# Kernel tuning notes

Measured on AMD Instinct MI355X. Metric: run time of the kernel, lower is better.

Reference implementation:

```python
import jax, jax.numpy as jnp
import numpy as np

NUM_BUCKETS = 32
MAX_DISTANCE = 128


def _relative_position_bucket(relative_position):
    # bidirectional=True variant of T5's bucketing
    n = -relative_position
    num_buckets = NUM_BUCKETS // 2
    ret = (n < 0).astype(jnp.int32) * num_buckets
    n = jnp.abs(n)
    max_exact = num_buckets // 2
    is_small = n < max_exact
    # log-spaced buckets for large distances
    val_if_large = max_exact + (
        jnp.log(jnp.maximum(n, 1).astype(jnp.float32) / max_exact)
        / np.log(MAX_DISTANCE / max_exact)
        * (num_buckets - max_exact)
    ).astype(jnp.int32)
    val_if_large = jnp.minimum(val_if_large, num_buckets - 1)
    return ret + jnp.where(is_small, n, val_if_large)


def setup_inputs() -> dict:
    key = jax.random.key(0)
    ks = jax.random.split(key, 6)
    B, S, D, H, DK = 4, 1024, 1024, 16, 64
    inner = H * DK
    s = 1.0 / np.sqrt(D).astype(np.float32)
    x = jax.random.normal(ks[0], (B, S, D), jnp.float32)
    Wq = jax.random.normal(ks[1], (D, inner), jnp.float32) * s
    Wk = jax.random.normal(ks[2], (D, inner), jnp.float32) * s
    Wv = jax.random.normal(ks[3], (D, inner), jnp.float32) * s
    Wo = jax.random.normal(ks[4], (inner, D), jnp.float32) * s
    rel_emb = jax.random.normal(ks[5], (NUM_BUCKETS, H), jnp.float32) * 0.02
    return {"x": x, "Wq": Wq, "Wk": Wk, "Wv": Wv, "Wo": Wo, "rel_emb": rel_emb}


def reference(x, Wq, Wk, Wv, Wo, rel_emb):
    B, S, D = x.shape
    H = rel_emb.shape[1]
    DK = Wq.shape[1] // H

    def shape_heads(t):  # [B,S,H*DK] -> [B,H,S,DK]
        return t.reshape(B, S, H, DK).transpose(0, 2, 1, 3)

    q = shape_heads(x @ Wq)
    k = shape_heads(x @ Wk)
    v = shape_heads(x @ Wv)

    # note: T5 does NOT scale by 1/sqrt(d_kv)
    scores = jnp.einsum("bhqd,bhkd->bhqk", q, k)

    pos = jnp.arange(S)
    rel = pos[None, :] - pos[:, None]            # memory - query
    bucket = _relative_position_bucket(rel)      # [S,S] int32
    bias = rel_emb[bucket].transpose(2, 0, 1)[None]  # [1,H,S,S]

    weights = jax.nn.softmax(scores + bias, axis=-1)
    ctx = jnp.einsum("bhqk,bhkd->bhqd", weights, v)
    ctx = ctx.transpose(0, 2, 1, 3).reshape(B, S, H * DK)
    return ctx @ Wo
```

## Files before the change

### kernel.cpp

```cpp
#include <hip/hip_runtime.h>
#include <math.h>

#define B_ 4
#define S_ 1024
#define D_ 1024
#define H_ 16
#define DK_ 64

typedef short bf16x8 __attribute__((ext_vector_type(8)));
typedef float f32x4 __attribute__((ext_vector_type(4)));

__device__ __forceinline__ unsigned short f2bf(float f) {
    unsigned int u = __float_as_uint(f);
    u = (u + 0x7FFFu + ((u >> 16) & 1u)) >> 16;
    return (unsigned short)u;
}

__device__ __forceinline__ float exp2_fast(float x) {
#if __has_builtin(__builtin_amdgcn_exp2f)
    return __builtin_amdgcn_exp2f(x);
#else
    return exp2f(x);
#endif
}

__device__ __forceinline__ int cvt_pk_bf16(float lo, float hi) {
    int r;
    asm("v_cvt_pk_bf16_f32 %0, %1, %2" : "=v"(r) : "v"(lo), "v"(hi));
    return r;
}

__device__ __forceinline__ void gl2lds16(const void* g, void* l) {
    typedef unsigned int u32;
    auto gp = (const __attribute__((address_space(1))) u32*)(unsigned long long)g;
    auto lp = (__attribute__((address_space(3))) u32*)(unsigned int)(unsigned long long)l;
    __builtin_amdgcn_global_load_lds(gp, lp, 16, 0, 0);
}

#define LOG2E 1.44269504f
#define BIAS_OFF 20.0f

__global__ __launch_bounds__(256) void conv_all(
    const float* __restrict__ x,
    const float* __restrict__ W0, const float* __restrict__ W1,
    const float* __restrict__ W2, const float* __restrict__ W3,
    unsigned short* __restrict__ xb, unsigned short* __restrict__ Wts)
{
    __shared__ float T[32][33];
    const int t = threadIdx.x;
    const int bid = blockIdx.x;

    if (bid < 4096) {
        int i = (bid * 256 + t) * 4;
        float4 v = *(const float4*)&x[i];
        ushort4 o;
        o.x = f2bf(v.x); o.y = f2bf(v.y); o.z = f2bf(v.z); o.w = f2bf(v.w);
        *(ushort4*)&xb[i] = o;
        return;
    }
    int tile = bid - 4096;
    const int mat = tile >> 10;
    tile &= 1023;
    const float* W = (mat == 0) ? W0 : (mat == 1) ? W1 : (mat == 2) ? W2 : W3;
    unsigned short* Wt = Wts + (size_t)mat * 1048576;
    const int k0 = (tile >> 5) * 32, n0 = (tile & 31) * 32;
    {
        int r = t >> 3, c4 = (t & 7) * 4;
        float4 v = *(const float4*)&W[(size_t)(k0 + r) * D_ + n0 + c4];
        T[r][c4 + 0] = v.x; T[r][c4 + 1] = v.y; T[r][c4 + 2] = v.z; T[r][c4 + 3] = v.w;
    }
    __syncthreads();
    {
        int rn = t >> 3, c4 = (t & 7) * 4;
        ushort4 o;
        o.x = f2bf(T[c4 + 0][rn]); o.y = f2bf(T[c4 + 1][rn]);
        o.z = f2bf(T[c4 + 2][rn]); o.w = f2bf(T[c4 + 3][rn]);
        *(ushort4*)&Wt[(size_t)(n0 + rn) * D_ + k0 + c4] = o;
    }
}

__global__ __launch_bounds__(256) void gemm_qkv(
    const unsigned short* __restrict__ xb,
    const unsigned short* __restrict__ Wts,
    unsigned short* __restrict__ Qb, unsigned short* __restrict__ Kb,
    unsigned short* __restrict__ Vtb)
{
    const int bid = blockIdx.x;
    const int by = bid & 31;
    const int t_ = bid >> 5;
    const int z = t_ >> 3;
    const int bx = t_ & 7;
    const unsigned short* Bt = Wts + (size_t)z * 1048576;

    __shared__ __align__(16) unsigned short Ast[2][128][32];
    __shared__ __align__(16) unsigned short Bst[2][128][32];

    const int tid = threadIdx.x;
    const int wave = tid >> 6, lane = tid & 63;
    const int quad = lane >> 4, l16 = lane & 15;
    const int wm = (wave & 1) * 64, wn = (wave >> 1) * 64;
    const int row0 = by * 128, col0 = bx * 128;
    const int lr = lane >> 2, lc = (lane & 3) * 8;

    f32x4 acc[4][4];
#pragma unroll
    for (int i = 0; i < 4; i++)
#pragma unroll
        for (int j = 0; j < 4; j++) acc[i][j] = 0;

    auto stage = [&](int sb, int k0) {
#pragma unroll
        for (int c = 0; c < 2; c++) {
            int m = wave * 32 + c * 16;
            gl2lds16(&xb[(size_t)(row0 + m + lr) * D_ + k0 + lc], &Ast[sb][m][0]);
            gl2lds16(&Bt[(size_t)(col0 + m + lr) * D_ + k0 + lc], &Bst[sb][m][0]);
        }
    };

    stage(0, 0);
    int db = 0;
    for (int k0 = 0; k0 < D_; k0 += 32) {
        __syncthreads();
        if (k0 + 32 < D_) stage(db ^ 1, k0 + 32);

        bf16x8 af[4], bfr[4];
#pragma unroll
        for (int mt = 0; mt < 4; mt++)
            af[mt] = *(const bf16x8*)&Ast[db][wm + mt * 16 + l16][quad * 8];
#pragma unroll
        for (int nt = 0; nt < 4; nt++)
            bfr[nt] = *(const bf16x8*)&Bst[db][wn + nt * 16 + l16][quad * 8];
#pragma unroll
        for (int mt = 0; mt < 4; mt++)
#pragma unroll
            for (int nt = 0; nt < 4; nt++)
                acc[mt][nt] = __builtin_amdgcn_mfma_f32_16x16x32_bf16(
                    af[mt], bfr[nt], acc[mt][nt], 0, 0, 0);
        db ^= 1;
    }

    const float scale = (z == 0) ? LOG2E : 1.0f;
#pragma unroll
    for (int mt = 0; mt < 4; mt++)
#pragma unroll
        for (int nt = 0; nt < 4; nt++)
#pragma unroll
            for (int reg = 0; reg < 4; reg++) {
                int row = row0 + wm + mt * 16 + quad * 4 + reg;
                int col = col0 + wn + nt * 16 + l16;
                int b = row >> 10, s = row & 1023;
                int h = col >> 6, dk = col & 63;
                unsigned short v = f2bf(acc[mt][nt][reg] * scale);
                if (z == 0)      Qb[(((size_t)(b * H_ + h)) * S_ + s) * DK_ + dk] = v;
                else if (z == 1) Kb[(((size_t)(b * H_ + h)) * S_ + s) * DK_ + dk] = v;
                else             Vtb[(((size_t)(b * H_ + h)) * DK_ + dk) * S_ + s] = v;
            }
}

__global__ __launch_bounds__(256) void gemm_out(
    const unsigned short* __restrict__ Ab,
    const unsigned short* __restrict__ Bt,
    float* __restrict__ out)
{
    const int bid = blockIdx.x;
    const int by = bid & 63;
    const int bx = bid >> 6;

    __shared__ __align__(16) unsigned short Ast[2][64][32];
    __shared__ __align__(16) unsigned short Bst[2][128][32];

    const int tid = threadIdx.x;
    const int wave = tid >> 6, lane = tid & 63;
    const int quad = lane >> 4, l16 = lane & 15;
    const int wm = (wave & 1) * 32, wn = (wave >> 1) * 64;
    const int row0 = by * 64, col0 = bx * 128;
    const int lr = lane >> 2, lc = (lane & 3) * 8;

    f32x4 acc[2][4];
#pragma unroll
    for (int i = 0; i < 2; i++)
#pragma unroll
        for (int j = 0; j < 4; j++) acc[i][j] = 0;

    auto stage = [&](int sb, int k0) {
        gl2lds16(&Ab[(size_t)(row0 + wave * 16 + lr) * D_ + k0 + lc],
                 &Ast[sb][wave * 16][0]);
#pragma unroll
        for (int c = 0; c < 2; c++) {
            int m = (wave * 2 + c) * 16;
            gl2lds16(&Bt[(size_t)(col0 + m + lr) * D_ + k0 + lc], &Bst[sb][m][0]);
        }
    };

    stage(0, 0);
    int db = 0;
    for (int k0 = 0; k0 < D_; k0 += 32) {
        __syncthreads();
        if (k0 + 32 < D_) stage(db ^ 1, k0 + 32);

        bf16x8 af[2], bfr[4];
#pragma unroll
        for (int mt = 0; mt < 2; mt++)
            af[mt] = *(const bf16x8*)&Ast[db][wm + mt * 16 + l16][quad * 8];
#pragma unroll
        for (int nt = 0; nt < 4; nt++)
            bfr[nt] = *(const bf16x8*)&Bst[db][wn + nt * 16 + l16][quad * 8];
#pragma unroll
        for (int mt = 0; mt < 2; mt++)
#pragma unroll
            for (int nt = 0; nt < 4; nt++)
                acc[mt][nt] = __builtin_amdgcn_mfma_f32_16x16x32_bf16(
                    af[mt], bfr[nt], acc[mt][nt], 0, 0, 0);
        db ^= 1;
    }

#pragma unroll
    for (int mt = 0; mt < 2; mt++)
#pragma unroll
        for (int nt = 0; nt < 4; nt++)
#pragma unroll
            for (int reg = 0; reg < 4; reg++) {
                int row = row0 + wm + mt * 16 + quad * 4 + reg;
                int col = col0 + wn + nt * 16 + l16;
                out[(size_t)row * D_ + col] = acc[mt][nt][reg];
            }
}

__global__ __launch_bounds__(256) void attn_mfma(
    const unsigned short* __restrict__ Qb, const unsigned short* __restrict__ Kb,
    const unsigned short* __restrict__ Vtb, const float* __restrict__ rel_emb,
    unsigned short* __restrict__ CTXb)
{
    __shared__ __align__(16) unsigned short Ks[2][64][64];
    __shared__ __align__(16) unsigned short Vts[2][64][64];
    __shared__ float bias_tab[2047];

    const int bid = blockIdx.x;
    const int bh = bid & 63;
    const int b = bh >> 4, h = bh & 15;
    const int q0 = (bid >> 6) * 128;
    const int tid = threadIdx.x;
    const int wave = tid >> 6, lane = tid & 63;
    const int quad = lane >> 4, l16 = lane & 15;
    const int qw = q0 + wave * 32;

    for (int idx = tid; idx < 2047; idx += 256) {
        int rel = idx - 1023;
        int n = -rel, ret = 0;
        if (n < 0) { ret = 16; n = -n; }
        int bkt;
        if (n < 8) bkt = ret + n;
        else {
            float t = logf((float)n / 8.0f) / logf(16.0f) * 8.0f;
            int v = 8 + (int)t;
            if (v > 15) v = 15;
            bkt = ret + v;
        }
        bias_tab[idx] = rel_emb[bkt * H_ + h] * LOG2E - BIAS_OFF;
    }

    const size_t hb = (size_t)(b * H_ + h) * (S_ * DK_);
    const unsigned short* Qp = Qb + hb;
    const unsigned short* Kp = Kb + hb;
    const unsigned short* Vp = Vtb + hb;

    bf16x8 qf[2][2];
#pragma unroll
    for (int sub = 0; sub < 2; sub++)
#pragma unroll
        for (int ks = 0; ks < 2; ks++)
            qf[sub][ks] = *(const bf16x8*)
                &Qp[(size_t)(qw + sub * 16 + l16) * DK_ + ks * 32 + quad * 8];

    f32x4 O[2][4];
#pragma unroll
    for (int sub = 0; sub < 2; sub++)
#pragma unroll
        for (int dt = 0; dt < 4; dt++) O[sub][dt] = 0;
    float lsum[2] = {0.f, 0.f};

    const int swz = l16 & 7;
    const int kr8 = lane >> 3;
    const int kck = ((lane & 7) ^ kr8) * 8;

    auto stageKV = [&](int db, int k0) {
#pragma unroll
        for (int i = 0; i < 2; i++) {
            int blk = wave * 2 + i;
            gl2lds16(&Kp[(size_t)(k0 + blk * 8 + kr8) * DK_ + kck],
                     &Ks[db][blk * 8][0]);
            gl2lds16(&Vp[(size_t)(blk * 8 + kr8) * S_ + k0 + kck],
                     &Vts[db][blk * 8][0]);
        }
    };

    stageKV(0, 0);

    for (int kt = 0; kt < 16; kt++) {
        const int k0 = kt * 64;
        const int db = kt & 1;
        __syncthreads();
        if (kt < 15) stageKV(db ^ 1, k0 + 64);

#pragma unroll
        for (int nt2 = 0; nt2 < 2; nt2++) {
            bf16x8 kf[2][2], vf[4];
#pragma unroll
            for (int t = 0; t < 2; t++) {
                int row = (2 * nt2 + t) * 16 + l16;
#pragma unroll
                for (int ks = 0; ks < 2; ks++)
                    kf[t][ks] = *(const bf16x8*)
                        &Ks[db][row][((ks * 4 + quad) ^ swz) * 8];
            }
#pragma unroll
            for (int dt = 0; dt < 4; dt++)
                vf[dt] = *(const bf16x8*)
                    &Vts[db][dt * 16 + l16][((nt2 * 4 + quad) ^ swz) * 8];

#pragma unroll
            for (int sub = 0; sub < 2; sub++) {
                f32x4 sacc[2];
#pragma unroll
                for (int t = 0; t < 2; t++) {
                    int b0 = 1023 + k0 + (2 * nt2 + t) * 16 + quad * 4
                             - (qw + sub * 16 + l16);
#pragma unroll
                    for (int reg = 0; reg < 4; reg++)
                        sacc[t][reg] = bias_tab[b0 + reg];
                }
                __builtin_amdgcn_s_setprio(1);
#pragma unroll
                for (int ks = 0; ks < 2; ks++)
#pragma unroll
                    for (int t = 0; t < 2; t++)
                        sacc[t] = __builtin_amdgcn_mfma_f32_16x16x32_bf16(
                            kf[t][ks], qf[sub][ks], sacc[t], 0, 0, 0);
                __builtin_amdgcn_s_setprio(0);

                float e0[4], e1[4];
#pragma unroll
                for (int reg = 0; reg < 4; reg++) {
                    e0[reg] = exp2_fast(sacc[0][reg]);
                    e1[reg] = exp2_fast(sacc[1][reg]);
                }
                lsum[sub] += (e0[0] + e0[1]) + (e0[2] + e0[3])
                           + (e1[0] + e1[1]) + (e1[2] + e1[3]);

                int x0 = cvt_pk_bf16(e0[0], e0[1]);
                int x1 = cvt_pk_bf16(e0[2], e0[3]);
                int x2 = cvt_pk_bf16(e1[0], e1[1]);
                int x3 = cvt_pk_bf16(e1[2], e1[3]);
                asm("v_permlane32_swap_b32 %0, %1" : "+v"(x0), "+v"(x2));
                asm("v_permlane32_swap_b32 %0, %1" : "+v"(x1), "+v"(x3));
                asm("v_permlane16_swap_b32 %0, %1" : "+v"(x0), "+v"(x2));
                asm("v_permlane16_swap_b32 %0, %1" : "+v"(x1), "+v"(x3));
                int4 pi; pi.x = x0; pi.y = x1; pi.z = x2; pi.w = x3;
                bf16x8 pf = __builtin_bit_cast(bf16x8, pi);

                __builtin_amdgcn_s_setprio(1);
#pragma unroll
                for (int dt = 0; dt < 4; dt++)
                    O[sub][dt] = __builtin_amdgcn_mfma_f32_16x16x32_bf16(
                        pf, vf[dt], O[sub][dt], 0, 0, 0);
                __builtin_amdgcn_s_setprio(0);
            }
        }
    }

#pragma unroll
    for (int sub = 0; sub < 2; sub++) {
        float l = lsum[sub];
        l += __shfl_xor(l, 16);
        l += __shfl_xor(l, 32);
        float invl = 1.0f / l;
#pragma unroll
        for (int reg = 0; reg < 4; reg++) {
            float inv = __shfl(invl, quad * 4 + reg);
            int s = qw + sub * 16 + quad * 4 + reg;
#pragma unroll
            for (int dt = 0; dt < 4; dt++) {
                int col = h * DK_ + dt * 16 + l16;
                CTXb[((size_t)(b * S_ + s)) * D_ + col] = f2bf(O[sub][dt][reg] * inv);
            }
        }
    }
}

extern "C" void kernel_launch(void* const* d_in, const int* in_sizes, int n_in,
                              void* d_out, int out_size, void* d_ws, size_t ws_size,
                              hipStream_t stream) {
    const float* x   = (const float*)d_in[0];
    const float* Wq  = (const float*)d_in[1];
    const float* Wk  = (const float*)d_in[2];
    const float* Wv  = (const float*)d_in[3];
    const float* Wo  = (const float*)d_in[4];
    const float* rel = (const float*)d_in[5];
    float* out = (float*)d_out;

    unsigned short* ws = (unsigned short*)d_ws;
    unsigned short* xb   = ws;
    unsigned short* Wts  = ws + (size_t)4194304;
    unsigned short* Qb   = ws + (size_t)8388608;
    unsigned short* Kb   = ws + (size_t)12582912;
    unsigned short* Vtb  = ws + (size_t)16777216;
    unsigned short* CTXb = ws + (size_t)20971520;

    conv_all<<<8192, 256, 0, stream>>>(x, Wq, Wk, Wv, Wo, xb, Wts);
    gemm_qkv<<<768, 256, 0, stream>>>(xb, Wts, Qb, Kb, Vtb);
    attn_mfma<<<512, 256, 0, stream>>>(Qb, Kb, Vtb, rel, CTXb);
    gemm_out<<<512, 256, 0, stream>>>(CTXb, Wts + (size_t)3 * 1048576, out);
}
```

Measured before the change: 169.8 us.

## Split attention key range across two blocks and add partial-combine kernel

The attention kernel now splits the 1024 keys into two halves, so twice as many blocks run, each covering 512 keys for a 128-query tile. Each block writes unnormalised fp32 partial outputs and row sums, and a new combine kernel adds the two halves, normalises, and converts to bf16 for the output GEMM. The per-block bias table shrinks to the range of relative positions that block actually needs. The aim is better CU occupancy and load balance, at the cost of extra fp32 global traffic for the partials and one more kernel launch.

```diff
diff --git a/kernel.cpp b/kernel.cpp
--- a/kernel.cpp
+++ b/kernel.cpp
@@ -229,23 +229,30 @@
 __global__ __launch_bounds__(256) void attn_mfma(
     const unsigned short* __restrict__ Qb, const unsigned short* __restrict__ Kb,
     const unsigned short* __restrict__ Vtb, const float* __restrict__ rel_emb,
-    unsigned short* __restrict__ CTXb)
+    float* __restrict__ O0, float* __restrict__ O1,
+    float* __restrict__ l0, float* __restrict__ l1)
 {
     __shared__ __align__(16) unsigned short Ks[2][64][64];
     __shared__ __align__(16) unsigned short Vts[2][64][64];
-    __shared__ float bias_tab[2047];
+    __shared__ float bias_tab[640];
 
     const int bid = blockIdx.x;
     const int bh = bid & 63;
     const int b = bh >> 4, h = bh & 15;
-    const int q0 = (bid >> 6) * 128;
+    const int rest = bid >> 6;
+    const int q0 = (rest & 7) * 128;
+    const int half = rest >> 3;
+    const int klo = half * 512;
+    float* __restrict__ Op = half ? O1 : O0;
+    float* __restrict__ Lp = half ? l1 : l0;
+
     const int tid = threadIdx.x;
     const int wave = tid >> 6, lane = tid & 63;
     const int quad = lane >> 4, l16 = lane & 15;
     const int qw = q0 + wave * 32;
 
-    for (int idx = tid; idx < 2047; idx += 256) {
-        int rel = idx - 1023;
+    for (int idx = tid; idx < 640; idx += 256) {
+        int rel = idx - 127 + klo - q0;
         int n = -rel, ret = 0;
         if (n < 0) { ret = 16; n = -n; }
         int bkt;
@@ -283,24 +290,24 @@
     const int kr8 = lane >> 3;
     const int kck = ((lane & 7) ^ kr8) * 8;
 
-    auto stageKV = [&](int db, int k0) {
+    auto stageKV = [&](int db, int kg) {
 #pragma unroll
         for (int i = 0; i < 2; i++) {
             int blk = wave * 2 + i;
-            gl2lds16(&Kp[(size_t)(k0 + blk * 8 + kr8) * DK_ + kck],
+            gl2lds16(&Kp[(size_t)(kg + blk * 8 + kr8) * DK_ + kck],
                      &Ks[db][blk * 8][0]);
-            gl2lds16(&Vp[(size_t)(blk * 8 + kr8) * S_ + k0 + kck],
+            gl2lds16(&Vp[(size_t)(blk * 8 + kr8) * S_ + kg + kck],
                      &Vts[db][blk * 8][0]);
         }
     };
 
-    stageKV(0, 0);
-
-    for (int kt = 0; kt < 16; kt++) {
-        const int k0 = kt * 64;
-        const int db = kt & 1;
+    stageKV(0, klo);
+
+    for (int ktl = 0; ktl < 8; ktl++) {
+        const int k0l = ktl * 64;
+        const int db = ktl & 1;
         __syncthreads();
-        if (kt < 15) stageKV(db ^ 1, k0 + 64);
+        if (ktl < 7) stageKV(db ^ 1, klo + k0l + 64);
 
 #pragma unroll
         for (int nt2 = 0; nt2 < 2; nt2++) {
@@ -323,8 +330,8 @@
                 f32x4 sacc[2];
 #pragma unroll
                 for (int t = 0; t < 2; t++) {
-                    int b0 = 1023 + k0 + (2 * nt2 + t) * 16 + quad * 4
-                             - (qw + sub * 16 + l16);
+                    int b0 = 127 + k0l + (2 * nt2 + t) * 16 + quad * 4
+                             - (wave * 32 + sub * 16 + l16);
 #pragma unroll
                     for (int reg = 0; reg < 4; reg++)
                         sacc[t][reg] = bias_tab[b0 + reg];
@@ -373,18 +380,41 @@
         float l = lsum[sub];
         l += __shfl_xor(l, 16);
         l += __shfl_xor(l, 32);
-        float invl = 1.0f / l;
+        if (quad == 0)
+            Lp[(size_t)(b * H_ + h) * S_ + qw + sub * 16 + l16] = l;
 #pragma unroll
         for (int reg = 0; reg < 4; reg++) {
-            float inv = __shfl(invl, quad * 4 + reg);
             int s = qw + sub * 16 + quad * 4 + reg;
 #pragma unroll
             for (int dt = 0; dt < 4; dt++) {
                 int col = h * DK_ + dt * 16 + l16;
-                CTXb[((size_t)(b * S_ + s)) * D_ + col] = f2bf(O[sub][dt][reg] * inv);
+                Op[((size_t)(b * S_ + s)) * D_ + col] = O[sub][dt][reg];
             }
         }
     }
+}
+
+__global__ __launch_bounds__(256) void combine_ctx(
+    const float* __restrict__ O0, const float* __restrict__ O1,
+    const float* __restrict__ l0, const float* __restrict__ l1,
+    unsigned short* __restrict__ CTXb)
+{
+    const int e = (blockIdx.x * 256 + threadIdx.x) * 8;
+    const int row = e >> 10;
+    const int col = e & 1023;
+    const int h = col >> 6;
+    const int lidx = ((row >> 10) * H_ + h) * S_ + (row & 1023);
+    const float inv = 1.0f / (l0[lidx] + l1[lidx]);
+    float4 a0 = *(const float4*)&O0[e];
+    float4 a1 = *(const float4*)&O1[e];
+    float4 c0 = *(const float4*)&O0[e + 4];
+    float4 c1 = *(const float4*)&O1[e + 4];
+    int4 o;
+    o.x = cvt_pk_bf16((a0.x + a1.x) * inv, (a0.y + a1.y) * inv);
+    o.y = cvt_pk_bf16((a0.z + a1.z) * inv, (a0.w + a1.w) * inv);
+    o.z = cvt_pk_bf16((c0.x + c1.x) * inv, (c0.y + c1.y) * inv);
+    o.w = cvt_pk_bf16((c0.z + c1.z) * inv, (c0.w + c1.w) * inv);
+    *(int4*)&CTXb[e] = o;
 }
 
 extern "C" void kernel_launch(void* const* d_in, const int* in_sizes, int n_in,
@@ -405,9 +435,14 @@
     unsigned short* Kb   = ws + (size_t)12582912;
     unsigned short* Vtb  = ws + (size_t)16777216;
     unsigned short* CTXb = ws + (size_t)20971520;
+    float* O0  = (float*)(ws + (size_t)25165824);
+    float* O1  = (float*)(ws + (size_t)33554432);
+    float* l0f = (float*)(ws + (size_t)41943040);
+    float* l1f = (float*)(ws + (size_t)42074112);
 
     conv_all<<<8192, 256, 0, stream>>>(x, Wq, Wk, Wv, Wo, xb, Wts);
     gemm_qkv<<<768, 256, 0, stream>>>(xb, Wts, Qb, Kb, Vtb);
-    attn_mfma<<<512, 256, 0, stream>>>(Qb, Kb, Vtb, rel, CTXb);
+    attn_mfma<<<1024, 256, 0, stream>>>(Qb, Kb, Vtb, rel, O0, O1, l0f, l1f);
+    combine_ctx<<<2048, 256, 0, stream>>>(O0, O1, l0f, l1f, CTXb);
     gemm_out<<<512, 256, 0, stream>>>(CTXb, Wts + (size_t)3 * 1048576, out);
 }
```

New measurement: 175.3 us. +3.2%, slower.

## Halve attention query tile to 64 rows and compute row sums via MFMA

Applied to the files above, without the earlier changes.

Each attention block now handles 64 queries instead of 128 (16 per wave), doubling the grid to 1024 blocks so more blocks are resident across CUs. The bias table is shrunk to cover only the relative-position range this block needs. The softmax denominator is now accumulated with an extra MFMA against a vector of bf16 ones rather than with VALU adds and cross-lane shuffles. In exchange, every K/V tile is loaded twice as often overall, and the row sum is taken from the bf16-rounded probabilities.

```diff
diff --git a/kernel.cpp b/kernel.cpp
--- a/kernel.cpp
+++ b/kernel.cpp
@@ -233,19 +233,19 @@
 {
     __shared__ __align__(16) unsigned short Ks[2][64][64];
     __shared__ __align__(16) unsigned short Vts[2][64][64];
-    __shared__ float bias_tab[2047];
+    __shared__ float bias_tab[1087];
 
     const int bid = blockIdx.x;
     const int bh = bid & 63;
     const int b = bh >> 4, h = bh & 15;
-    const int q0 = (bid >> 6) * 128;
+    const int q0 = (bid >> 6) * 64;
     const int tid = threadIdx.x;
     const int wave = tid >> 6, lane = tid & 63;
     const int quad = lane >> 4, l16 = lane & 15;
-    const int qw = q0 + wave * 32;
-
-    for (int idx = tid; idx < 2047; idx += 256) {
-        int rel = idx - 1023;
+    const int qw = q0 + wave * 16;
+
+    for (int idx = tid; idx < 1087; idx += 256) {
+        int rel = idx - 63 - q0;
         int n = -rel, ret = 0;
         if (n < 0) { ret = 16; n = -n; }
         int bkt;
@@ -264,33 +264,33 @@
     const unsigned short* Kp = Kb + hb;
     const unsigned short* Vp = Vtb + hb;
 
-    bf16x8 qf[2][2];
-#pragma unroll
-    for (int sub = 0; sub < 2; sub++)
-#pragma unroll
-        for (int ks = 0; ks < 2; ks++)
-            qf[sub][ks] = *(const bf16x8*)
-                &Qp[(size_t)(qw + sub * 16 + l16) * DK_ + ks * 32 + quad * 8];
-
-    f32x4 O[2][4];
-#pragma unroll
-    for (int sub = 0; sub < 2; sub++)
-#pragma unroll
-        for (int dt = 0; dt < 4; dt++) O[sub][dt] = 0;
-    float lsum[2] = {0.f, 0.f};
+    bf16x8 qf[2];
+#pragma unroll
+    for (int ks = 0; ks < 2; ks++)
+        qf[ks] = *(const bf16x8*)&Qp[(size_t)(qw + l16) * DK_ + ks * 32 + quad * 8];
+
+    bf16x8 onesf;
+#pragma unroll
+    for (int j = 0; j < 8; j++) onesf[j] = (short)0x3F80;
+
+    f32x4 O[4];
+#pragma unroll
+    for (int dt = 0; dt < 4; dt++) O[dt] = 0;
+    f32x4 lacc;
+    lacc = 0;
 
     const int swz = l16 & 7;
     const int kr8 = lane >> 3;
     const int kck = ((lane & 7) ^ kr8) * 8;
 
-    auto stageKV = [&](int db, int k0) {
+    auto stageKV = [&](int sb, int kg) {
 #pragma unroll
         for (int i = 0; i < 2; i++) {
             int blk = wave * 2 + i;
-            gl2lds16(&Kp[(size_t)(k0 + blk * 8 + kr8) * DK_ + kck],
-                     &Ks[db][blk * 8][0]);
-            gl2lds16(&Vp[(size_t)(blk * 8 + kr8) * S_ + k0 + kck],
-                     &Vts[db][blk * 8][0]);
+            gl2lds16(&Kp[(size_t)(kg + blk * 8 + kr8) * DK_ + kck],
+                     &Ks[sb][blk * 8][0]);
+            gl2lds16(&Vp[(size_t)(blk * 8 + kr8) * S_ + kg + kck],
+                     &Vts[sb][blk * 8][0]);
         }
     };
 
@@ -318,71 +318,61 @@
                 vf[dt] = *(const bf16x8*)
                     &Vts[db][dt * 16 + l16][((nt2 * 4 + quad) ^ swz) * 8];
 
-#pragma unroll
-            for (int sub = 0; sub < 2; sub++) {
-                f32x4 sacc[2];
-#pragma unroll
-                for (int t = 0; t < 2; t++) {
-                    int b0 = 1023 + k0 + (2 * nt2 + t) * 16 + quad * 4
-                             - (qw + sub * 16 + l16);
-#pragma unroll
-                    for (int reg = 0; reg < 4; reg++)
-                        sacc[t][reg] = bias_tab[b0 + reg];
-                }
-                __builtin_amdgcn_s_setprio(1);
-#pragma unroll
-                for (int ks = 0; ks < 2; ks++)
-#pragma unroll
-                    for (int t = 0; t < 2; t++)
-                        sacc[t] = __builtin_amdgcn_mfma_f32_16x16x32_bf16(
-                            kf[t][ks], qf[sub][ks], sacc[t], 0, 0, 0);
-                __builtin_amdgcn_s_setprio(0);
-
-                float e0[4], e1[4];
-#pragma unroll
-                for (int reg = 0; reg < 4; reg++) {
-                    e0[reg] = exp2_fast(sacc[0][reg]);
-                    e1[reg] = exp2_fast(sacc[1][reg]);
-                }
-                lsum[sub] += (e0[0] + e0[1]) + (e0[2] + e0[3])
-                           + (e1[0] + e1[1]) + (e1[2] + e1[3]);
-
-                int x0 = cvt_pk_bf16(e0[0], e0[1]);
-                int x1 = cvt_pk_bf16(e0[2], e0[3]);
-                int x2 = cvt_pk_bf16(e1[0], e1[1]);
-                int x3 = cvt_pk_bf16(e1[2], e1[3]);
-                asm("v_permlane32_swap_b32 %0, %1" : "+v"(x0), "+v"(x2));
-                asm("v_permlane32_swap_b32 %0, %1" : "+v"(x1), "+v"(x3));
-                asm("v_permlane16_swap_b32 %0, %1" : "+v"(x0), "+v"(x2));
-                asm("v_permlane16_swap_b32 %0, %1" : "+v"(x1), "+v"(x3));
-                int4 pi; pi.x = x0; pi.y = x1; pi.z = x2; pi.w = x3;
-                bf16x8 pf = __builtin_bit_cast(bf16x8, pi);
-
-                __builtin_amdgcn_s_setprio(1);
-#pragma unroll
-                for (int dt = 0; dt < 4; dt++)
-                    O[sub][dt] = __builtin_amdgcn_mfma_f32_16x16x32_bf16(
-                        pf, vf[dt], O[sub][dt], 0, 0, 0);
-                __builtin_amdgcn_s_setprio(0);
+            f32x4 sacc[2];
+#pragma unroll
+            for (int t = 0; t < 2; t++) {
+                int b0 = 63 + k0 + (2 * nt2 + t) * 16 + quad * 4
+                         - wave * 16 - l16;
+#pragma unroll
+                for (int reg = 0; reg < 4; reg++)
+                    sacc[t][reg] = bias_tab[b0 + reg];
             }
-        }
-    }
-
-#pragma unroll
-    for (int sub = 0; sub < 2; sub++) {
-        float l = lsum[sub];
-        l += __shfl_xor(l, 16);
-        l += __shfl_xor(l, 32);
-        float invl = 1.0f / l;
-#pragma unroll
-        for (int reg = 0; reg < 4; reg++) {
-            float inv = __shfl(invl, quad * 4 + reg);
-            int s = qw + sub * 16 + quad * 4 + reg;
-#pragma unroll
-            for (int dt = 0; dt < 4; dt++) {
-                int col = h * DK_ + dt * 16 + l16;
-                CTXb[((size_t)(b * S_ + s)) * D_ + col] = f2bf(O[sub][dt][reg] * inv);
+            __builtin_amdgcn_s_setprio(1);
+#pragma unroll
+            for (int ks = 0; ks < 2; ks++)
+#pragma unroll
+                for (int t = 0; t < 2; t++)
+                    sacc[t] = __builtin_amdgcn_mfma_f32_16x16x32_bf16(
+                        kf[t][ks], qf[ks], sacc[t], 0, 0, 0);
+            __builtin_amdgcn_s_setprio(0);
+
+            float e0[4], e1[4];
+#pragma unroll
+            for (int reg = 0; reg < 4; reg++) {
+                e0[reg] = exp2_fast(sacc[0][reg]);
+                e1[reg] = exp2_fast(sacc[1][reg]);
             }
+
+            int x0 = cvt_pk_bf16(e0[0], e0[1]);
+            int x1 = cvt_pk_bf16(e0[2], e0[3]);
+            int x2 = cvt_pk_bf16(e1[0], e1[1]);
+            int x3 = cvt_pk_bf16(e1[2], e1[3]);
+            asm("v_permlane32_swap_b32 %0, %1" : "+v"(x0), "+v"(x2));
+            asm("v_permlane32_swap_b32 %0, %1" : "+v"(x1), "+v"(x3));
+            asm("v_permlane16_swap_b32 %0, %1" : "+v"(x0), "+v"(x2));
+            asm("v_permlane16_swap_b32 %0, %1" : "+v"(x1), "+v"(x3));
+            int4 pi; pi.x = x0; pi.y = x1; pi.z = x2; pi.w = x3;
+            bf16x8 pf = __builtin_bit_cast(bf16x8, pi);
+
+            __builtin_amdgcn_s_setprio(1);
+#pragma unroll
+            for (int dt = 0; dt < 4; dt++)
+                O[dt] = __builtin_amdgcn_mfma_f32_16x16x32_bf16(
+                    pf, vf[dt], O[dt], 0, 0, 0);
+            lacc = __builtin_amdgcn_mfma_f32_16x16x32_bf16(
+                pf, onesf, lacc, 0, 0, 0);
+            __builtin_amdgcn_s_setprio(0);
+        }
+    }
+
+#pragma unroll
+    for (int reg = 0; reg < 4; reg++) {
+        float inv = 1.0f / lacc[reg];
+        int s = qw + quad * 4 + reg;
+#pragma unroll
+        for (int dt = 0; dt < 4; dt++) {
+            int col = h * DK_ + dt * 16 + l16;
+            CTXb[((size_t)(b * S_ + s)) * D_ + col] = f2bf(O[dt][reg] * inv);
         }
     }
 }
@@ -408,6 +398,6 @@
 
     conv_all<<<8192, 256, 0, stream>>>(x, Wq, Wk, Wv, Wo, xb, Wts);
     gemm_qkv<<<768, 256, 0, stream>>>(xb, Wts, Qb, Kb, Vtb);
-    attn_mfma<<<512, 256, 0, stream>>>(Qb, Kb, Vtb, rel, CTXb);
+    attn_mfma<<<1024, 256, 0, stream>>>(Qb, Kb, Vtb, rel, CTXb);
     gemm_out<<<512, 256, 0, stream>>>(CTXb, Wts + (size_t)3 * 1048576, out);
 }
```

Result: no change. 167.1 us (-1.6%).
